# Performance work log

Hardware: AMD Instinct MI355X
Metric: run time of the kernel (lower is better)

The kernel has to match this reference:

```python
import jax, jax.numpy as jnp
import numpy as np

SR = 22050
N_SAMPLES = 131072
N_FRAMES = 256
WS = 2048
STEP = WS // 2
C = 32
K = WS // 2 + 1
N_LAYERS = 3
B = 4
SPF = N_SAMPLES // N_FRAMES  # samples per frame = 512


def _morlet(M, w, s):
    # scipy.signal.morlet (complete=True)
    x = np.linspace(-s * 2 * np.pi, s * 2 * np.pi, M)
    return (np.exp(1j * w * x) - np.exp(-0.5 * w ** 2)) * np.exp(-0.5 * x ** 2) * np.pi ** -0.25


def _make_filter_bank():
    # musical_scale_hz(21, 129, K)
    midi = np.linspace(21.0, 129.0, K)
    hz = 440.0 * 2.0 ** ((midi - 69.0) / 12.0)
    basis = np.zeros((K, WS), dtype=np.complex128)
    s = 0.025
    for i, f in enumerate(hz):
        w = f / (s * 2 * SR / WS)
        basis[i] = _morlet(WS, w, s)
    basis = basis.real
    basis = basis / (np.linalg.norm(basis, axis=-1, keepdims=True) + 1e-8)
    # abs(rfft(fb, norm='ortho'))
    spec = np.abs(np.fft.rfft(basis, axis=-1) / np.sqrt(WS))
    return jnp.asarray(spec, dtype=jnp.float32)  # (K, K)


def _hann():
    # torch.hann_window default is periodic
    return 0.5 - 0.5 * jnp.cos(2.0 * jnp.pi * jnp.arange(WS) / WS)


def _windowed_audio(x):
    # pad right by step, unfold into overlapping frames, apply hann window
    xp = jnp.pad(x, ((0, 0), (0, 0), (0, STEP)))
    nf = (xp.shape[-1] - WS) // STEP + 1  # = 128
    idx = jnp.arange(nf)[:, None] * STEP + jnp.arange(WS)[None, :]
    frames = xp[..., idx]  # (B, C, F, WS)
    return frames * _hann()


def _overlap_add(frames):
    # apply_window=True: hann at synthesis, hop = WS//2
    x = frames * _hann()
    b, c, f, w = x.shape
    hop = w // 2
    first = x[..., :hop].reshape(b, c, f * hop)
    second = x[..., hop:].reshape(b, c, f * hop)
    return jnp.pad(first, ((0, 0), (0, 0), (0, hop))) + jnp.pad(second, ((0, 0), (0, 0), (hop, 0)))


def _fft_convolve(a, b):
    n = a.shape[-1]
    pa = [(0, 0)] * (a.ndim - 1) + [(0, n)]
    pb = [(0, 0)] * (b.ndim - 1) + [(0, n)]
    spec = jnp.fft.rfft(jnp.pad(a, pa), axis=-1) * jnp.fft.rfft(jnp.pad(b, pb), axis=-1)
    return jnp.fft.irfft(spec, axis=-1)[..., :n]


def _block(x, transfer, mixer_mat, gain, filter_bank):
    t = x.shape[-1]
    x = jnp.einsum('bct,cd->bdt', x, mixer_mat)  # channel mixing
    frames = _windowed_audio(x)                  # (B, C, F, WS)
    spec = jnp.fft.rfft(frames, axis=-1)         # (B, C, F, K) complex
    T = (transfer @ filter_bank).astype(spec.dtype)  # (C, K)
    spec_f = jnp.moveaxis(spec, 2, 0)            # (F, B, C, K)
    init = jnp.zeros(spec_f.shape[1:], dtype=spec.dtype)

    def step(carry, s):
        out = (s + carry) * T
        return out, out

    _, outs = jax.lax.scan(step, init, spec_f)   # linear recurrence over frames
    out = jnp.moveaxis(outs, 0, 2)               # (B, C, F, K)
    wins = jnp.fft.irfft(out, axis=-1)           # (B, C, F, WS)
    samples = _overlap_add(wins)
    samples = jnp.tanh(samples * gain[None, :, None])
    return samples[..., :t]


def _network(x, transfers, mixer_mats, gains, mixer, filter_bank):
    outputs = [x]
    inp = x
    for i in range(N_LAYERS):
        inp = _block(inp, transfers[i], mixer_mats[i], gains[i], filter_bank)
        outputs.append(inp)
    result = jnp.stack(outputs, axis=-1)         # (B, C, T, L+1)
    w = jax.nn.softmax(mixer)
    mixed = (result * w).sum(-1)                 # mixture over layer outputs
    return mixed.sum(axis=1, keepdims=True)      # (B, 1, T)


def setup_inputs() -> dict:
    key = jax.random.key(0)
    ks = jax.random.split(key, 8)
    sig = jax.random.uniform(ks[0], (B, C, N_FRAMES), dtype=jnp.float32) * 1e-2
    noise = jax.random.uniform(ks[1], (N_SAMPLES,), minval=-1.0, maxval=1.0, dtype=jnp.float32)
    channel_decays = jax.random.uniform(ks[2], (C,), dtype=jnp.float32)
    mixer = jax.random.normal(ks[3], (N_LAYERS + 1,), dtype=jnp.float32)
    res = jax.random.uniform(ks[4], (N_LAYERS, C, K), minval=0.5, maxval=0.9998, dtype=jnp.float32)
    mask = (jax.random.uniform(ks[5], (N_LAYERS, C, K)) < 0.01).astype(jnp.float32)
    transfers = res * mask                       # sparse resonances (p=0.01)
    mixer_mats = jnp.tile(jnp.eye(C, dtype=jnp.float32)[None], (N_LAYERS, 1, 1))
    gains = jax.random.uniform(ks[6], (N_LAYERS, C), minval=1.0, maxval=50.0, dtype=jnp.float32)
    filter_bank = _make_filter_bank()
    return dict(sig=sig, noise=noise, channel_decays=channel_decays, mixer=mixer,
                transfers=transfers, mixer_mats=mixer_mats, gains=gains, filter_bank=filter_bank)


def reference(sig, noise, channel_decays, mixer, transfers, mixer_mats, gains, filter_bank):
    # upsample_with_holes
    us = jnp.zeros((sig.shape[0], C, N_SAMPLES), dtype=sig.dtype).at[..., ::SPF].set(sig)
    # per-channel decaying envelopes
    ls = jnp.linspace(1.0, 0.0, SPF, dtype=sig.dtype)[None, None, :] ** channel_decays[None, :, None]
    ls = jnp.pad(ls, ((0, 0), (0, 0), (0, N_SAMPLES - SPF)))
    us = _fft_convolve(us, ls) * noise
    result = _network(us, transfers, mixer_mats, gains, mixer, filter_bank)
    return result, sig
```

## Files before the change

### kernel.cpp

```cpp
#include <hip/hip_runtime.h>
#include <math.h>

constexpr int BB   = 4;
constexpr int CC   = 32;
constexpr int TT   = 131072;
constexpr int NFRM = 128;
constexpr int KK   = 1025;
constexpr int HOP  = 1024;
constexpr int SPF  = 512;
constexpr int SIGF = 256;
constexpr int NL   = 3;
constexpr int RST  = 2052;
constexpr int NBC  = BB*CC;
constexpr int NROWS = NBC*NFRM;
constexpr int MAXNZ = 256;
constexpr int GRP  = 8;
constexpr int FPG  = 16;

#define PD4(a) ((a) + ((a) >> 3))

__device__ __forceinline__ float4 f4add(float4 a, float4 b){return make_float4(a.x+b.x,a.y+b.y,a.z+b.z,a.w+b.w);}
__device__ __forceinline__ float4 f4sub(float4 a, float4 b){return make_float4(a.x-b.x,a.y-b.y,a.z-b.z,a.w-b.w);}
__device__ __forceinline__ float4 cmul4(float4 v, float c, float s){
  return make_float4(v.x*c - v.y*s, v.x*s + v.y*c, v.z*c - v.w*s, v.z*s + v.w*c);
}

template<int SGN>
__device__ __forceinline__ void dft4p(float4 v[4]) {
  float4 b0=f4add(v[0],v[2]), b1=f4sub(v[0],v[2]), b2=f4add(v[1],v[3]), b3=f4sub(v[1],v[3]);
  float4 ib3 = (SGN<0)? make_float4(b3.y,-b3.x,b3.w,-b3.z) : make_float4(-b3.y,b3.x,-b3.w,b3.z);
  v[0]=f4add(b0,b2); v[2]=f4sub(b0,b2);
  v[1]=f4add(b1,ib3); v[3]=f4sub(b1,ib3);
}

template<int SGN, bool FINAL_STORE>
__device__ __forceinline__ void stockham_pp(float4 v[4], float4* S4a, float4* S4b, int tid) {
  int pb = 0;
  #pragma unroll
  for (int Ns=1; Ns<1024; Ns*=4) {
    if (Ns>1) {
      int k = tid & (Ns-1);
      float ang = (float)SGN * 6.28318530717958647692f * (float)k / (float)(4*Ns);
      float s1,c1; __sincosf(ang,&s1,&c1);
      float c2=c1*c1-s1*s1, s2=2.f*c1*s1;
      float c3=c2*c1-s2*s1, s3=c2*s1+s2*c1;
      v[1]=cmul4(v[1],c1,s1); v[2]=cmul4(v[2],c2,s2); v[3]=cmul4(v[3],c3,s3);
    }
    dft4p<SGN>(v);
    if (Ns<256 || FINAL_STORE) {
      float4* B = (pb == 0) ? S4a : S4b;
      pb ^= 1;
      int idxD = ((tid & ~(Ns-1))<<2) | (tid & (Ns-1));
      B[PD4(idxD       )] = v[0];
      B[PD4(idxD +   Ns)] = v[1];
      B[PD4(idxD + 2*Ns)] = v[2];
      B[PD4(idxD + 3*Ns)] = v[3];
      __syncthreads();
      if (Ns<256) {
        v[0]=B[PD4(tid)]; v[1]=B[PD4(tid+256)]; v[2]=B[PD4(tid+512)]; v[3]=B[PD4(tid+768)];
      }
    }
  }
}

template<int SGN, bool FINAL_STORE>
__device__ __forceinline__ void stockham_sb(float4 v[4], float4* S4, int tid) {
  #pragma unroll
  for (int Ns=1; Ns<1024; Ns*=4) {
    if (Ns>1) {
      int k = tid & (Ns-1);
      float ang = (float)SGN * 6.28318530717958647692f * (float)k / (float)(4*Ns);
      float s1,c1; __sincosf(ang,&s1,&c1);
      float c2=c1*c1-s1*s1, s2=2.f*c1*s1;
      float c3=c2*c1-s2*s1, s3=c2*s1+s2*c1;
      v[1]=cmul4(v[1],c1,s1); v[2]=cmul4(v[2],c2,s2); v[3]=cmul4(v[3],c3,s3);
    }
    dft4p<SGN>(v);
    if (Ns<256 || FINAL_STORE) {
      int idxD = ((tid & ~(Ns-1))<<2) | (tid & (Ns-1));
      S4[PD4(idxD       )] = v[0];
      S4[PD4(idxD +   Ns)] = v[1];
      S4[PD4(idxD + 2*Ns)] = v[2];
      S4[PD4(idxD + 3*Ns)] = v[3];
      __syncthreads();
      if (Ns<256) {
        v[0]=S4[PD4(tid)]; v[1]=S4[PD4(tid+256)]; v[2]=S4[PD4(tid+512)]; v[3]=S4[PD4(tid+768)];
        __syncthreads();
      }
    }
  }
}

__global__ void k_tables(const float* __restrict__ decay, float* __restrict__ ENVt,
                         float* __restrict__ HANN, float* __restrict__ PKt,
                         float* __restrict__ UPKt) {
  int gid = blockIdx.x*256 + threadIdx.x;
  if (gid < CC*SPF) {
    int c = gid >> 9, r = gid & 511;
    float d = decay[c];
    float env;
    if (r == 511) env = (d == 0.f) ? 1.f : 0.f;
    else          env = powf((float)(511-r)*(1.0f/511.0f), d);
    ENVt[gid] = env;
  }
  if (gid < 2048) HANN[gid] = 0.5f - 0.5f*cosf((float)gid*(float)(M_PI/1024.0));
  if (gid <= 1024) { float s,c; sincosf(-(float)M_PI*(float)gid*(1.0f/1024.0f),&s,&c); PKt[2*gid]=c; PKt[2*gid+1]=s; }
  if (gid <  1024) { float s,c; sincosf( (float)M_PI*(float)gid*(1.0f/1024.0f),&s,&c); UPKt[2*gid]=c; UPKt[2*gid+1]=s; }
}

__global__ void __launch_bounds__(64) k_nnz(const float* __restrict__ tr,
    int* __restrict__ NZI, float* __restrict__ NZV, int* __restrict__ NZC) {
  int lc = blockIdx.x;
  int lane = threadIdx.x;
  const float* trow = tr + (size_t)lc*KK;
  int base = 0;
  for (int start = 0; start < KK; start += 64) {
    int kp = start + lane;
    float v = (kp < KK) ? trow[kp] : 0.f;
    unsigned long long m = __ballot(v != 0.f);
    int pos = base + __popcll(m & ((1ull<<lane)-1ull));
    if (v != 0.f && pos < MAXNZ) { NZI[lc*MAXNZ+pos] = kp; NZV[lc*MAXNZ+pos] = v; }
    base += __popcll(m);
  }
  if (lane == 0) NZC[lc] = (base < MAXNZ) ? base : MAXNZ;
}

__global__ void __launch_bounds__(256) k_tmat2(const int* __restrict__ NZI,
    const float* __restrict__ NZV, const int* __restrict__ NZC,
    const float* __restrict__ fb, float* __restrict__ TM) {
  int gid = blockIdx.x*256 + threadIdx.x;
  if (gid >= NL*CC*KK) return;
  int k = gid % KK, lc = gid / KK;
  int n = NZC[lc];
  const int*   zi = NZI + lc*MAXNZ;
  const float* zv = NZV + lc*MAXNZ;
  float acc = 0.f;
  for (int i = 0; i < n; ++i)
    acc = fmaf(zv[i], fb[(size_t)zi[i]*KK + k], acc);
  TM[gid] = acc;
}

__global__ void k_ident(const float* __restrict__ mats, int* __restrict__ FLG) {
  int l = blockIdx.x;
  const float* M = mats + (size_t)l*CC*CC;
  __shared__ int ok;
  if (threadIdx.x == 0) ok = 1;
  __syncthreads();
  for (int i = threadIdx.x; i < CC*CC; i += 256) {
    float ex = ((i>>5) == (i&31)) ? 1.f : 0.f;
    if (M[i] != ex) ok = 0;
  }
  __syncthreads();
  if (threadIdx.x == 0) FLG[l] = ok;
}

__global__ void __launch_bounds__(256) k_us_init(const float* __restrict__ sig,
    const float* __restrict__ noise, const float* __restrict__ mixer,
    const float* __restrict__ M0, const float* __restrict__ ENVt,
    float* __restrict__ X, float* __restrict__ out) {
  __shared__ float sM[CC*CC];
  int tid = threadIdx.x;
  for (int i = tid; i < CC*CC; i += 256) sM[i] = M0[i];
  __syncthreads();
  int gid = blockIdx.x*256 + tid;
  int b = gid >> 17, t = gid & (TT-1);
  int q = t >> 9, r = t & 511;
  float nz = noise[t];
  float u[CC]; float s = 0.f;
  #pragma unroll
  for (int c = 0; c < CC; ++c) { u[c] = sig[(b*CC+c)*SIGF + q] * ENVt[c*SPF + r]; s += u[c]; }
  float m0=mixer[0],m1=mixer[1],m2=mixer[2],m3=mixer[3];
  float mx=fmaxf(fmaxf(m0,m1),fmaxf(m2,m3));
  float e0=__expf(m0-mx),e1=__expf(m1-mx),e2=__expf(m2-mx),e3=__expf(m3-mx);
  float w0=e0/(e0+e1+e2+e3);
  out[gid] = w0 * nz * s;
  #pragma unroll
  for (int d = 0; d < CC; ++d) {
    float acc = 0.f;
    #pragma unroll
    for (int c = 0; c < CC; ++c) acc = fmaf(u[c], sM[c*CC+d], acc);
    X[(size_t)(b*CC+d)*TT + t] = nz * acc;
  }
  if (gid < BB*CC*SIGF) out[BB*TT + gid] = sig[gid];
}

__global__ void __launch_bounds__(256) k_mix_cond(float* __restrict__ X,
    const float* __restrict__ M, const int* __restrict__ FLG, int layer) {
  if (FLG[layer]) return;
  __shared__ float sM[CC*CC];
  int tid = threadIdx.x;
  for (int i = tid; i < CC*CC; i += 256) sM[i] = M[i];
  __syncthreads();
  int gid = blockIdx.x*256 + tid;
  int b = gid >> 17, t = gid & (TT-1);
  float* xp = X + (size_t)b*CC*TT + t;
  float xv[CC];
  #pragma unroll
  for (int c = 0; c < CC; ++c) xv[c] = xp[(size_t)c*TT];
  for (int d = 0; d < CC; ++d) {
    float acc = 0.f;
    #pragma unroll
    for (int c = 0; c < CC; ++c) acc = fmaf(xv[c], sM[c*CC+d], acc);
    xp[(size_t)d*TT] = acc;
  }
}

__global__ void __launch_bounds__(256) k_fwd_scan(const float* __restrict__ X,
    float* __restrict__ SPEC, float* __restrict__ EB, const float* __restrict__ TM,
    const float* __restrict__ HANN, const float* __restrict__ PKt) {
  __shared__ float4 S4a[1152];
  __shared__ float4 S4b[1152];
  int tid = threadIdx.x;
  int blk = blockIdx.x;
  int g = blk & (GRP-1), bc = blk >> 3;
  int c = bc & (CC-1);
  const float* xr = X + (size_t)bc*TT;
  float Tv[5]; float2 cr[5];
  #pragma unroll
  for (int j = 0; j < 5; ++j) {
    int k = tid + 256*j;
    Tv[j] = (k <= 1024) ? TM[c*KK + k] : 0.f;
    cr[j] = make_float2(0.f, 0.f);
  }
  float2 inA[4], inB[4];
  {
    int s0 = g*FPG*HOP;
    #pragma unroll
    for (int r = 0; r < 4; ++r) {
      int n = tid + 256*r;
      inA[r] = *(const float2*)(xr + s0 + 2*n);
      int sb = s0 + HOP + 2*n;
      inB[r] = (sb < TT) ? *(const float2*)(xr + sb) : make_float2(0.f,0.f);
    }
  }
  for (int p = 0; p < FPG/2; ++p) {
    int f0 = g*FPG + 2*p;
    float4 v[4];
    #pragma unroll
    for (int r = 0; r < 4; ++r) {
      int n = tid + 256*r;
      float2 h = *(const float2*)(HANN + 2*n);
      v[r] = make_float4(inA[r].x*h.x, inA[r].y*h.y, inB[r].x*h.x, inB[r].y*h.y);
    }
    if (p < FPG/2 - 1) {
      int s0 = (f0 + 2)*HOP;
      #pragma unroll
      for (int r = 0; r < 4; ++r) {
        int n = tid + 256*r;
        inA[r] = *(const float2*)(xr + s0 + 2*n);
        int sb = s0 + HOP + 2*n;
        inB[r] = (sb < TT) ? *(const float2*)(xr + sb) : make_float2(0.f,0.f);
      }
    }
    stockham_pp<-1, true>(v, S4a, S4b, tid);
    float* row0 = SPEC + (size_t)(bc*NFRM + f0)*RST;
    float* row1 = row0 + RST;
    #pragma unroll
    for (int j = 0; j < 5; ++j) {
      int k = tid + 256*j;
      if (k <= 1024) {
        float4 Zk = S4a[PD4(k & 1023)];
        float4 Zm = S4a[PD4((1024-k) & 1023)];
        float2 pk = *(const float2*)(PKt + 2*k);
        float zex = 0.5f*(Zk.x+Zm.x), zey = 0.5f*(Zk.y-Zm.y);
        float zox = 0.5f*(Zk.y+Zm.y), zoy = -0.5f*(Zk.x-Zm.x);
        float sax = zex + pk.x*zox - pk.y*zoy;
        float say = zey + pk.x*zoy + pk.y*zox;
        zex = 0.5f*(Zk.z+Zm.z); zey = 0.5f*(Zk.w-Zm.w);
        zox = 0.5f*(Zk.w+Zm.w); zoy = -0.5f*(Zk.z-Zm.z);
        float sbx = zex + pk.x*zox - pk.y*zoy;
        float sby = zey + pk.x*zoy + pk.y*zox;
        cr[j].x = (sax + cr[j].x)*Tv[j];
        cr[j].y = (say + cr[j].y)*Tv[j];
        *(float2*)(row0 + 2*k) = cr[j];
        cr[j].x = (sbx + cr[j].x)*Tv[j];
        cr[j].y = (sby + cr[j].y)*Tv[j];
        *(float2*)(row1 + 2*k) = cr[j];
      }
    }
    __syncthreads();
  }
  float* er = EB + (size_t)blk*RST;
  #pragma unroll
  for (int j = 0; j < 5; ++j) {
    int k = tid + 256*j;
    if (k <= 1024) *(float2*)(er + 2*k) = cr[j];
  }
}

__global__ void __launch_bounds__(256) k_carry(float* __restrict__ EB, const float* __restrict__ TM) {
  int gid = blockIdx.x*256 + threadIdx.x;
  if (gid >= NBC*KK) return;
  int bc = gid / KK, k = gid - bc*KK;
  int c = bc & (CC-1);
  float T = TM[c*KK + k];
  float t2 = T*T, t4 = t2*t2, t8 = t4*t4, T16 = t8*t8;
  float2 cc = make_float2(0.f, 0.f);
  for (int g = 0; g < GRP; ++g) {
    float* p = EB + (size_t)(bc*GRP + g)*RST + 2*k;
    float2 e = *(float2*)p;
    *(float2*)p = cc;
    cc.x = e.x + T16*cc.x;
    cc.y = e.y + T16*cc.y;
  }
}

__global__ void __launch_bounds__(256) k_inv_ola(const float* __restrict__ SPEC,
    const float* __restrict__ EB, const float* __restrict__ TM,
    const float* __restrict__ HANN, const float* __restrict__ UPKt,
    const float* __restrict__ gains, float* __restrict__ X) {
  __shared__ float4 S4[1152];
  int tid = threadIdx.x;
  int blk = blockIdx.x;
  int g = blk & (GRP-1), bc = blk >> 3;
  int c = bc & (CC-1);
  int fb = g*FPG;
  float sg = gains[c];
  const float* ec = EB + (size_t)blk*RST;
  float Tn[4], Tm[4]; float2 dN[4], dM[4];
  #pragma unroll
  for (int r = 0; r < 4; ++r) {
    int n = tid + 256*r, m = 1024 - n;
    Tn[r] = TM[c*KK + n]; Tm[r] = TM[c*KK + m];
    dN[r] = *(const float2*)(ec + 2*n);
    dM[r] = *(const float2*)(ec + 2*m);
  }
  float2 pAn[4], pAm[4];
  float2 pr0 = make_float2(0.f,0.f), pr1 = make_float2(0.f,0.f);
  float* xw = X + (size_t)bc*TT;
  const float sc = 1.0f/1024.0f;
  for (int rnd = 0; rnd <= FPG/2; ++rnd) {
    float4 v[4];
    #pragma unroll
    for (int r = 0; r < 4; ++r) {
      int n = tid + 256*r, m = 1024 - n;
      float2 An, Am, Bn, Bm;
      if (rnd == 0) { An = dN[r]; Am = dM[r]; }
      else {
        dN[r].x *= Tn[r]; dN[r].y *= Tn[r];
        dM[r].x *= Tm[r]; dM[r].y *= Tm[r];
        An = make_float2(pAn[r].x + dN[r].x, pAn[r].y + dN[r].y);
        Am = make_float2(pAm[r].x + dM[r].x, pAm[r].y + dM[r].y);
      }
      if (rnd < FPG/2) {
        const float* rowB = SPEC + (size_t)(bc*NFRM + fb + 2*rnd)*RST;
        float2 a  = *(const float2*)(rowB + 2*n);
        float2 bv = *(const float2*)(rowB + 2*m);
        dN[r].x *= Tn[r]; dN[r].y *= Tn[r];
        dM[r].x *= Tm[r]; dM[r].y *= Tm[r];
        Bn = make_float2(a.x + dN[r].x, a.y + dN[r].y);
        Bm = make_float2(bv.x + dM[r].x, bv.y + dM[r].y);
      } else { Bn = make_float2(0.f,0.f); Bm = make_float2(0.f,0.f); }
      float2 u = *(const float2*)(UPKt + 2*n);
      float zex = 0.5f*(An.x+Am.x), zey = 0.5f*(An.y-Am.y);
      float dx  = 0.5f*(An.x-Am.x), dy  = 0.5f*(An.y+Am.y);
      float zox = u.x*dx - u.y*dy, zoy = u.x*dy + u.y*dx;
      v[r].x = zex - zoy; v[r].y = zey + zox;
      zex = 0.5f*(Bn.x+Bm.x); zey = 0.5f*(Bn.y-Bm.y);
      dx  = 0.5f*(Bn.x-Bm.x); dy  = 0.5f*(Bn.y+Bm.y);
      zox = u.x*dx - u.y*dy; zoy = u.x*dy + u.y*dx;
      v[r].z = zex - zoy; v[r].w = zey + zox;
    }
    if (rnd < FPG/2) {
      const float* rowA = SPEC + (size_t)(bc*NFRM + fb + 2*rnd + 1)*RST;
      #pragma unroll
      for (int r = 0; r < 4; ++r) {
        int n = tid + 256*r, m = 1024 - n;
        pAn[r] = *(const float2*)(rowA + 2*n);
        pAm[r] = *(const float2*)(rowA + 2*m);
      }
    }
    stockham_sb<1, false>(v, S4, tid);
    #pragma unroll
    for (int r = 0; r < 4; ++r) {
      int n = tid + 256*r;
      float2 h = *(const float2*)(HANN + 2*n);
      v[r].x *= sc*h.x; v[r].y *= sc*h.y;
      v[r].z *= sc*h.x; v[r].w *= sc*h.y;
    }
    if (rnd >= 1) {
      int tbase = (fb + 2*rnd - 1)*HOP;
      float2 o0 = make_float2(tanhf(sg*(v[0].x + pr0.x)), tanhf(sg*(v[0].y + pr0.y)));
      float2 o1 = make_float2(tanhf(sg*(v[1].x + pr1.x)), tanhf(sg*(v[1].y + pr1.y)));
      *(float2*)(xw + tbase + 2*tid)        = o0;
      *(float2*)(xw + tbase + 2*(tid+256))  = o1;
    }
    if (rnd < FPG/2) {
      int tbase = (fb + 2*rnd)*HOP;
      float2 o0 = make_float2(tanhf(sg*(v[0].z + v[2].x)), tanhf(sg*(v[0].w + v[2].y)));
      float2 o1 = make_float2(tanhf(sg*(v[1].z + v[3].x)), tanhf(sg*(v[1].w + v[3].y)));
      *(float2*)(xw + tbase + 2*tid)        = o0;
      *(float2*)(xw + tbase + 2*(tid+256))  = o1;
      pr0 = make_float2(v[2].z, v[2].w);
      pr1 = make_float2(v[3].z, v[3].w);
    }
  }
}

__global__ void __launch_bounds__(256) k_out(const float* __restrict__ X,
    const float* __restrict__ mixer, int layer, float* __restrict__ out) {
  int gid = blockIdx.x*256 + threadIdx.x;
  int t4 = gid*4;
  int b = t4 >> 17, t = t4 & (TT-1);
  float m0=mixer[0],m1=mixer[1],m2=mixer[2],m3=mixer[3];
  float mx=fmaxf(fmaxf(m0,m1),fmaxf(m2,m3));
  float e[4]={__expf(m0-mx),__expf(m1-mx),__expf(m2-mx),__expf(m3-mx)};
  float w = e[layer+1]/(e[0]+e[1]+e[2]+e[3]);
  float4 acc = make_float4(0.f,0.f,0.f,0.f);
  #pragma unroll
  for (int c = 0; c < CC; ++c) {
    float4 xv = *(const float4*)(X + (size_t)(b*CC+c)*TT + t);
    acc.x += xv.x; acc.y += xv.y; acc.z += xv.z; acc.w += xv.w;
  }
  float4 o = *(float4*)(out + t4);
  o.x += w*acc.x; o.y += w*acc.y; o.z += w*acc.z; o.w += w*acc.w;
  *(float4*)(out + t4) = o;
}

extern "C" void kernel_launch(void* const* d_in, const int* in_sizes, int n_in,
                              void* d_out, int out_size, void* d_ws, size_t ws_size,
                              hipStream_t stream) {
  const float* sig        = (const float*)d_in[0];
  const float* noise      = (const float*)d_in[1];
  const float* decay      = (const float*)d_in[2];
  const float* mixer      = (const float*)d_in[3];
  const float* transfers  = (const float*)d_in[4];
  const float* mixer_mats = (const float*)d_in[5];
  const float* gains      = (const float*)d_in[6];
  const float* fb         = (const float*)d_in[7];
  float* out = (float*)d_out;
  float* ws  = (float*)d_ws;

  float* X    = ws;
  float* SPEC = X + (size_t)16777216;
  float* EB   = SPEC + (size_t)NROWS*RST;
  float* TM   = EB + (size_t)NBC*GRP*RST;
  float* ENVt = TM + (size_t)NL*CC*KK;
  float* HANN = ENVt + CC*SPF;
  float* PKt  = HANN + 2048;
  float* UPKt = PKt + 2050;
  float* NZVf = UPKt + 2048;
  int*   NZI  = (int*)(NZVf + NL*CC*MAXNZ);
  int*   NZC  = NZI + NL*CC*MAXNZ;
  int*   FLG  = NZC + NL*CC;

  k_tables<<<64, 256, 0, stream>>>(decay, ENVt, HANN, PKt, UPKt);
  k_nnz<<<NL*CC, 64, 0, stream>>>(transfers, NZI, NZVf, NZC);
  k_tmat2<<<(NL*CC*KK + 255)/256, 256, 0, stream>>>(NZI, NZVf, NZC, fb, TM);
  k_ident<<<NL, 256, 0, stream>>>(mixer_mats, FLG);
  k_us_init<<<BB*TT/256, 256, 0, stream>>>(sig, noise, mixer, mixer_mats, ENVt, X, out);

  for (int l = 0; l < NL; ++l) {
    const float* TMl = TM + (size_t)l*CC*KK;
    if (l > 0)
      k_mix_cond<<<BB*TT/256, 256, 0, stream>>>(X, mixer_mats + (size_t)l*CC*CC, FLG, l);
    k_fwd_scan<<<NBC*GRP, 256, 0, stream>>>(X, SPEC, EB, TMl, HANN, PKt);
    k_carry<<<(NBC*KK + 255)/256, 256, 0, stream>>>(EB, TMl);
    k_inv_ola<<<NBC*GRP, 256, 0, stream>>>(SPEC, EB, TMl, HANN, UPKt, gains + (size_t)l*CC, X);
    k_out<<<BB*TT/1024, 256, 0, stream>>>(X, mixer, l, out);
  }
}
```

Measured before the change: 528.0 us.

## Split inverse OLA scan into half-groups to double block parallelism

Each inverse-FFT/overlap-add block now processes 8 frames instead of 16, doubling the grid. Second-half blocks reconstruct their starting recursion state by scaling the group carry by T^8 and preloading the preceding spectrum row. This raises occupancy and parallelism at the cost of one extra FFT round per block and redundant loads.

```diff
diff --git a/kernel.cpp b/kernel.cpp
--- a/kernel.cpp
+++ b/kernel.cpp
@@ -16,6 +16,8 @@
 constexpr int MAXNZ = 256;
 constexpr int GRP  = 8;
 constexpr int FPG  = 16;
+constexpr int GI   = 16;
+constexpr int FI   = 8;
 
 #define PD4(a) ((a) + ((a) >> 3))
 
@@ -312,11 +314,12 @@
   __shared__ float4 S4[1152];
   int tid = threadIdx.x;
   int blk = blockIdx.x;
-  int g = blk & (GRP-1), bc = blk >> 3;
+  int g2 = blk & (GI-1), bc = blk >> 4;
+  int half = g2 & 1;
   int c = bc & (CC-1);
-  int fb = g*FPG;
+  int fb = g2*FI;
   float sg = gains[c];
-  const float* ec = EB + (size_t)blk*RST;
+  const float* ec = EB + (size_t)((bc<<3) | (g2>>1))*RST;
   float Tn[4], Tm[4]; float2 dN[4], dM[4];
   #pragma unroll
   for (int r = 0; r < 4; ++r) {
@@ -324,25 +327,43 @@
     Tn[r] = TM[c*KK + n]; Tm[r] = TM[c*KK + m];
     dN[r] = *(const float2*)(ec + 2*n);
     dM[r] = *(const float2*)(ec + 2*m);
+    if (half) {
+      float a2=Tn[r]*Tn[r], a4=a2*a2, a8=a4*a4;
+      float b2=Tm[r]*Tm[r], b4=b2*b2, b8=b4*b4;
+      dN[r].x *= a8; dN[r].y *= a8;
+      dM[r].x *= b8; dM[r].y *= b8;
+    }
   }
   float2 pAn[4], pAm[4];
+  if (half) {
+    const float* rowP = SPEC + (size_t)(bc*NFRM + fb - 1)*RST;
+    #pragma unroll
+    for (int r = 0; r < 4; ++r) {
+      int n = tid + 256*r, m = 1024 - n;
+      pAn[r] = *(const float2*)(rowP + 2*n);
+      pAm[r] = *(const float2*)(rowP + 2*m);
+    }
+  }
   float2 pr0 = make_float2(0.f,0.f), pr1 = make_float2(0.f,0.f);
   float* xw = X + (size_t)bc*TT;
   const float sc = 1.0f/1024.0f;
-  for (int rnd = 0; rnd <= FPG/2; ++rnd) {
+  for (int rnd = 0; rnd <= FI/2; ++rnd) {
     float4 v[4];
     #pragma unroll
     for (int r = 0; r < 4; ++r) {
       int n = tid + 256*r, m = 1024 - n;
       float2 An, Am, Bn, Bm;
-      if (rnd == 0) { An = dN[r]; Am = dM[r]; }
-      else {
+      if (rnd == 0) {
+        if (half) { An = make_float2(pAn[r].x + dN[r].x, pAn[r].y + dN[r].y);
+                    Am = make_float2(pAm[r].x + dM[r].x, pAm[r].y + dM[r].y); }
+        else      { An = dN[r]; Am = dM[r]; }
+      } else {
         dN[r].x *= Tn[r]; dN[r].y *= Tn[r];
         dM[r].x *= Tm[r]; dM[r].y *= Tm[r];
         An = make_float2(pAn[r].x + dN[r].x, pAn[r].y + dN[r].y);
         Am = make_float2(pAm[r].x + dM[r].x, pAm[r].y + dM[r].y);
       }
-      if (rnd < FPG/2) {
+      if (rnd < FI/2) {
         const float* rowB = SPEC + (size_t)(bc*NFRM + fb + 2*rnd)*RST;
         float2 a  = *(const float2*)(rowB + 2*n);
         float2 bv = *(const float2*)(rowB + 2*m);
@@ -361,7 +382,7 @@
       zox = u.x*dx - u.y*dy; zoy = u.x*dy + u.y*dx;
       v[r].z = zex - zoy; v[r].w = zey + zox;
     }
-    if (rnd < FPG/2) {
+    if (rnd < FI/2) {
       const float* rowA = SPEC + (size_t)(bc*NFRM + fb + 2*rnd + 1)*RST;
       #pragma unroll
       for (int r = 0; r < 4; ++r) {
@@ -385,7 +406,7 @@
       *(float2*)(xw + tbase + 2*tid)        = o0;
       *(float2*)(xw + tbase + 2*(tid+256))  = o1;
     }
-    if (rnd < FPG/2) {
+    if (rnd < FI/2) {
       int tbase = (fb + 2*rnd)*HOP;
       float2 o0 = make_float2(tanhf(sg*(v[0].z + v[2].x)), tanhf(sg*(v[0].w + v[2].y)));
       float2 o1 = make_float2(tanhf(sg*(v[1].z + v[3].x)), tanhf(sg*(v[1].w + v[3].y)));
@@ -456,7 +477,7 @@
       k_mix_cond<<<BB*TT/256, 256, 0, stream>>>(X, mixer_mats + (size_t)l*CC*CC, FLG, l);
     k_fwd_scan<<<NBC*GRP, 256, 0, stream>>>(X, SPEC, EB, TMl, HANN, PKt);
     k_carry<<<(NBC*KK + 255)/256, 256, 0, stream>>>(EB, TMl);
-    k_inv_ola<<<NBC*GRP, 256, 0, stream>>>(SPEC, EB, TMl, HANN, UPKt, gains + (size_t)l*CC, X);
+    k_inv_ola<<<NBC*GI, 256, 0, stream>>>(SPEC, EB, TMl, HANN, UPKt, gains + (size_t)l*CC, X);
     k_out<<<BB*TT/1024, 256, 0, stream>>>(X, mixer, l, out);
   }
 }
```

New measurement: 575.3 us. 1.09x slower.

## Batch four frames per inverse FFT pass to halve barrier count in inverse OLA

Applied to the files above, without the earlier changes.

The inverse OLA kernel now builds two packed complex FFT inputs (four frames) per iteration and runs them through a dual Stockham routine that shares barriers and twiddle computation, with a tail pass handling the last frame. This cuts the number of __syncthreads and loop iterations per frame group. It also doubles shared memory and adds a min-blocks launch bound of 4, which raises register pressure and may cause spills or limit occupancy.

```diff
diff --git a/kernel.cpp b/kernel.cpp
--- a/kernel.cpp
+++ b/kernel.cpp
@@ -89,6 +89,40 @@
       }
     }
   }
+}
+
+template<int SGN>
+__device__ __forceinline__ void stockham_dual(float4 v[4], float4 w[4],
+                                              float4* A, float4* B, int tid) {
+  #pragma unroll
+  for (int Ns=1; Ns<1024; Ns*=4) {
+    if (Ns>1) {
+      int k = tid & (Ns-1);
+      float ang = (float)SGN * 6.28318530717958647692f * (float)k / (float)(4*Ns);
+      float s1,c1; __sincosf(ang,&s1,&c1);
+      float c2=c1*c1-s1*s1, s2=2.f*c1*s1;
+      float c3=c2*c1-s2*s1, s3=c2*s1+s2*c1;
+      v[1]=cmul4(v[1],c1,s1); v[2]=cmul4(v[2],c2,s2); v[3]=cmul4(v[3],c3,s3);
+      w[1]=cmul4(w[1],c1,s1); w[2]=cmul4(w[2],c2,s2); w[3]=cmul4(w[3],c3,s3);
+    }
+    dft4p<SGN>(v); dft4p<SGN>(w);
+    if (Ns<256) {
+      int idxD = ((tid & ~(Ns-1))<<2) | (tid & (Ns-1));
+      A[PD4(idxD)]=v[0]; A[PD4(idxD+Ns)]=v[1]; A[PD4(idxD+2*Ns)]=v[2]; A[PD4(idxD+3*Ns)]=v[3];
+      B[PD4(idxD)]=w[0]; B[PD4(idxD+Ns)]=w[1]; B[PD4(idxD+2*Ns)]=w[2]; B[PD4(idxD+3*Ns)]=w[3];
+      __syncthreads();
+      v[0]=A[PD4(tid)]; v[1]=A[PD4(tid+256)]; v[2]=A[PD4(tid+512)]; v[3]=A[PD4(tid+768)];
+      w[0]=B[PD4(tid)]; w[1]=B[PD4(tid+256)]; w[2]=B[PD4(tid+512)]; w[3]=B[PD4(tid+768)];
+      __syncthreads();
+    }
+  }
+}
+
+__device__ __forceinline__ float2 unpk(float2 Sn, float2 Sm, float2 u) {
+  float zex = 0.5f*(Sn.x+Sm.x), zey = 0.5f*(Sn.y-Sm.y);
+  float dx  = 0.5f*(Sn.x-Sm.x), dy  = 0.5f*(Sn.y+Sm.y);
+  float zox = u.x*dx - u.y*dy, zoy = u.x*dy + u.y*dx;
+  return make_float2(zex - zoy, zey + zox);
 }
 
 __global__ void k_tables(const float* __restrict__ decay, float* __restrict__ ENVt,
@@ -305,11 +339,12 @@
   }
 }
 
-__global__ void __launch_bounds__(256) k_inv_ola(const float* __restrict__ SPEC,
+__global__ void __launch_bounds__(256, 4) k_inv_ola(const float* __restrict__ SPEC,
     const float* __restrict__ EB, const float* __restrict__ TM,
     const float* __restrict__ HANN, const float* __restrict__ UPKt,
     const float* __restrict__ gains, float* __restrict__ X) {
-  __shared__ float4 S4[1152];
+  __shared__ float4 A4[1152];
+  __shared__ float4 B4[1152];
   int tid = threadIdx.x;
   int blk = blockIdx.x;
   int g = blk & (GRP-1), bc = blk >> 3;
@@ -325,75 +360,117 @@
     dN[r] = *(const float2*)(ec + 2*n);
     dM[r] = *(const float2*)(ec + 2*m);
   }
-  float2 pAn[4], pAm[4];
   float2 pr0 = make_float2(0.f,0.f), pr1 = make_float2(0.f,0.f);
   float* xw = X + (size_t)bc*TT;
   const float sc = 1.0f/1024.0f;
-  for (int rnd = 0; rnd <= FPG/2; ++rnd) {
-    float4 v[4];
+  for (int rr = 0; rr < 4; ++rr) {
+    int q0 = fb - 1 + 4*rr;
+    float4 v[4], w[4];
     #pragma unroll
     for (int r = 0; r < 4; ++r) {
       int n = tid + 256*r, m = 1024 - n;
-      float2 An, Am, Bn, Bm;
-      if (rnd == 0) { An = dN[r]; Am = dM[r]; }
+      float2 u = *(const float2*)(UPKt + 2*n);
+      float2 S0n, S0m, S1n, S1m;
+      if (rr == 0) { S0n = dN[r]; S0m = dM[r]; }
       else {
         dN[r].x *= Tn[r]; dN[r].y *= Tn[r];
         dM[r].x *= Tm[r]; dM[r].y *= Tm[r];
-        An = make_float2(pAn[r].x + dN[r].x, pAn[r].y + dN[r].y);
-        Am = make_float2(pAm[r].x + dM[r].x, pAm[r].y + dM[r].y);
-      }
-      if (rnd < FPG/2) {
-        const float* rowB = SPEC + (size_t)(bc*NFRM + fb + 2*rnd)*RST;
-        float2 a  = *(const float2*)(rowB + 2*n);
-        float2 bv = *(const float2*)(rowB + 2*m);
+        const float* rw = SPEC + (size_t)(bc*NFRM + q0)*RST;
+        float2 a = *(const float2*)(rw + 2*n), b = *(const float2*)(rw + 2*m);
+        S0n = make_float2(a.x + dN[r].x, a.y + dN[r].y);
+        S0m = make_float2(b.x + dM[r].x, b.y + dM[r].y);
+      }
+      {
         dN[r].x *= Tn[r]; dN[r].y *= Tn[r];
         dM[r].x *= Tm[r]; dM[r].y *= Tm[r];
-        Bn = make_float2(a.x + dN[r].x, a.y + dN[r].y);
-        Bm = make_float2(bv.x + dM[r].x, bv.y + dM[r].y);
-      } else { Bn = make_float2(0.f,0.f); Bm = make_float2(0.f,0.f); }
-      float2 u = *(const float2*)(UPKt + 2*n);
-      float zex = 0.5f*(An.x+Am.x), zey = 0.5f*(An.y-Am.y);
-      float dx  = 0.5f*(An.x-Am.x), dy  = 0.5f*(An.y+Am.y);
-      float zox = u.x*dx - u.y*dy, zoy = u.x*dy + u.y*dx;
-      v[r].x = zex - zoy; v[r].y = zey + zox;
-      zex = 0.5f*(Bn.x+Bm.x); zey = 0.5f*(Bn.y-Bm.y);
-      dx  = 0.5f*(Bn.x-Bm.x); dy  = 0.5f*(Bn.y+Bm.y);
-      zox = u.x*dx - u.y*dy; zoy = u.x*dy + u.y*dx;
-      v[r].z = zex - zoy; v[r].w = zey + zox;
-    }
-    if (rnd < FPG/2) {
-      const float* rowA = SPEC + (size_t)(bc*NFRM + fb + 2*rnd + 1)*RST;
-      #pragma unroll
-      for (int r = 0; r < 4; ++r) {
-        int n = tid + 256*r, m = 1024 - n;
-        pAn[r] = *(const float2*)(rowA + 2*n);
-        pAm[r] = *(const float2*)(rowA + 2*m);
-      }
-    }
-    stockham_sb<1, false>(v, S4, tid);
+        const float* rw = SPEC + (size_t)(bc*NFRM + q0 + 1)*RST;
+        float2 a = *(const float2*)(rw + 2*n), b = *(const float2*)(rw + 2*m);
+        S1n = make_float2(a.x + dN[r].x, a.y + dN[r].y);
+        S1m = make_float2(b.x + dM[r].x, b.y + dM[r].y);
+      }
+      float2 p0 = unpk(S0n, S0m, u), p1 = unpk(S1n, S1m, u);
+      v[r] = make_float4(p0.x, p0.y, p1.x, p1.y);
+      {
+        dN[r].x *= Tn[r]; dN[r].y *= Tn[r];
+        dM[r].x *= Tm[r]; dM[r].y *= Tm[r];
+        const float* rw = SPEC + (size_t)(bc*NFRM + q0 + 2)*RST;
+        float2 a = *(const float2*)(rw + 2*n), b = *(const float2*)(rw + 2*m);
+        S0n = make_float2(a.x + dN[r].x, a.y + dN[r].y);
+        S0m = make_float2(b.x + dM[r].x, b.y + dM[r].y);
+      }
+      {
+        dN[r].x *= Tn[r]; dN[r].y *= Tn[r];
+        dM[r].x *= Tm[r]; dM[r].y *= Tm[r];
+        const float* rw = SPEC + (size_t)(bc*NFRM + q0 + 3)*RST;
+        float2 a = *(const float2*)(rw + 2*n), b = *(const float2*)(rw + 2*m);
+        S1n = make_float2(a.x + dN[r].x, a.y + dN[r].y);
+        S1m = make_float2(b.x + dM[r].x, b.y + dM[r].y);
+      }
+      p0 = unpk(S0n, S0m, u); p1 = unpk(S1n, S1m, u);
+      w[r] = make_float4(p0.x, p0.y, p1.x, p1.y);
+    }
+    stockham_dual<1>(v, w, A4, B4, tid);
     #pragma unroll
     for (int r = 0; r < 4; ++r) {
       int n = tid + 256*r;
       float2 h = *(const float2*)(HANN + 2*n);
-      v[r].x *= sc*h.x; v[r].y *= sc*h.y;
-      v[r].z *= sc*h.x; v[r].w *= sc*h.y;
-    }
-    if (rnd >= 1) {
-      int tbase = (fb + 2*rnd - 1)*HOP;
+      v[r].x *= sc*h.x; v[r].y *= sc*h.y; v[r].z *= sc*h.x; v[r].w *= sc*h.y;
+      w[r].x *= sc*h.x; w[r].y *= sc*h.y; w[r].z *= sc*h.x; w[r].w *= sc*h.y;
+    }
+    if (rr >= 1) {
+      int tb = q0*HOP;
       float2 o0 = make_float2(tanhf(sg*(v[0].x + pr0.x)), tanhf(sg*(v[0].y + pr0.y)));
       float2 o1 = make_float2(tanhf(sg*(v[1].x + pr1.x)), tanhf(sg*(v[1].y + pr1.y)));
-      *(float2*)(xw + tbase + 2*tid)        = o0;
-      *(float2*)(xw + tbase + 2*(tid+256))  = o1;
-    }
-    if (rnd < FPG/2) {
-      int tbase = (fb + 2*rnd)*HOP;
+      *(float2*)(xw + tb + 2*tid)       = o0;
+      *(float2*)(xw + tb + 2*(tid+256)) = o1;
+    }
+    {
+      int tb = (q0+1)*HOP;
       float2 o0 = make_float2(tanhf(sg*(v[0].z + v[2].x)), tanhf(sg*(v[0].w + v[2].y)));
       float2 o1 = make_float2(tanhf(sg*(v[1].z + v[3].x)), tanhf(sg*(v[1].w + v[3].y)));
-      *(float2*)(xw + tbase + 2*tid)        = o0;
-      *(float2*)(xw + tbase + 2*(tid+256))  = o1;
-      pr0 = make_float2(v[2].z, v[2].w);
-      pr1 = make_float2(v[3].z, v[3].w);
-    }
+      *(float2*)(xw + tb + 2*tid)       = o0;
+      *(float2*)(xw + tb + 2*(tid+256)) = o1;
+    }
+    {
+      int tb = (q0+2)*HOP;
+      float2 o0 = make_float2(tanhf(sg*(w[0].x + v[2].z)), tanhf(sg*(w[0].y + v[2].w)));
+      float2 o1 = make_float2(tanhf(sg*(w[1].x + v[3].z)), tanhf(sg*(w[1].y + v[3].w)));
+      *(float2*)(xw + tb + 2*tid)       = o0;
+      *(float2*)(xw + tb + 2*(tid+256)) = o1;
+    }
+    {
+      int tb = (q0+3)*HOP;
+      float2 o0 = make_float2(tanhf(sg*(w[0].z + w[2].x)), tanhf(sg*(w[0].w + w[2].y)));
+      float2 o1 = make_float2(tanhf(sg*(w[1].z + w[3].x)), tanhf(sg*(w[1].w + w[3].y)));
+      *(float2*)(xw + tb + 2*tid)       = o0;
+      *(float2*)(xw + tb + 2*(tid+256)) = o1;
+    }
+    pr0 = make_float2(w[2].z, w[2].w);
+    pr1 = make_float2(w[3].z, w[3].w);
+  }
+  {
+    float4 v[4];
+    #pragma unroll
+    for (int r = 0; r < 4; ++r) {
+      int n = tid + 256*r, m = 1024 - n;
+      float2 u = *(const float2*)(UPKt + 2*n);
+      dN[r].x *= Tn[r]; dN[r].y *= Tn[r];
+      dM[r].x *= Tm[r]; dM[r].y *= Tm[r];
+      const float* rw = SPEC + (size_t)(bc*NFRM + fb + 15)*RST;
+      float2 a = *(const float2*)(rw + 2*n), b = *(const float2*)(rw + 2*m);
+      float2 Sn = make_float2(a.x + dN[r].x, a.y + dN[r].y);
+      float2 Sm = make_float2(b.x + dM[r].x, b.y + dM[r].y);
+      float2 p0 = unpk(Sn, Sm, u);
+      v[r] = make_float4(p0.x, p0.y, 0.f, 0.f);
+    }
+    stockham_sb<1, false>(v, A4, tid);
+    int tb = (fb+15)*HOP;
+    float2 h0 = *(const float2*)(HANN + 2*tid);
+    float2 h1 = *(const float2*)(HANN + 2*(tid+256));
+    float2 o0 = make_float2(tanhf(sg*(v[0].x*sc*h0.x + pr0.x)), tanhf(sg*(v[0].y*sc*h0.y + pr0.y)));
+    float2 o1 = make_float2(tanhf(sg*(v[1].x*sc*h1.x + pr1.x)), tanhf(sg*(v[1].y*sc*h1.y + pr1.y)));
+    *(float2*)(xw + tb + 2*tid)       = o0;
+    *(float2*)(xw + tb + 2*(tid+256)) = o1;
   }
 }
 
```

Measured after the change: 925.1 us. 1.75x slower.
